# Kernel optimization log

Hardware: AMD Instinct MI355X
Metric: run time of the kernel (lower is better)

Reference implementation:

```python
import jax, jax.numpy as jnp
import numpy as np

EPS = 1e-5  # torch BatchNorm1d default eps


def _bn(x, gamma, beta):
    # training-mode batch norm over axis 0 (biased variance, like torch)
    m = x.mean(axis=0)
    v = x.var(axis=0)
    return (x - m) * jax.lax.rsqrt(v + EPS) * gamma + beta


def setup_inputs() -> dict:
    key = jax.random.key(0)
    ks = jax.random.split(key, 6)
    B, T, D_IN, E, H, D_OUT = 8192, 64, 2, 128, 128, 5
    s = 0.05
    f32 = jnp.float32
    return {
        "inputs": jax.random.normal(ks[0], (B, T, D_IN), f32),
        # input BatchNorm1d(2)
        "in_gamma": jnp.ones((D_IN,), f32),
        "in_beta": jnp.zeros((D_IN,), f32),
        # input embed MLP: Linear(2->128) + BN(128) + ReLU
        "W_emb": jax.random.normal(ks[1], (E, D_IN), f32) * s,
        "b_emb": jnp.zeros((E,), f32),
        "emb_gamma": jnp.ones((E,), f32),
        "emb_beta": jnp.zeros((E,), f32),
        # LSTMCell(128, 128): gate order i, f, g, o
        "W_ih": jax.random.normal(ks[2], (4 * H, E), f32) * s,
        "W_hh": jax.random.normal(ks[3], (4 * H, H), f32) * s,
        "b_ih": jnp.zeros((4 * H,), f32),
        "b_hh": jnp.zeros((4 * H,), f32),
        # output MLP: Linear(128->5) + BN(5), no activation
        "W_out": jax.random.normal(ks[4], (D_OUT, H), f32) * s,
        "b_out": jnp.zeros((D_OUT,), f32),
        "out_gamma": jnp.ones((D_OUT,), f32),
        "out_beta": jnp.zeros((D_OUT,), f32),
    }


def reference(inputs, in_gamma, in_beta, W_emb, b_emb, emb_gamma, emb_beta,
              W_ih, W_hh, b_ih, b_hh, W_out, b_out, out_gamma, out_beta):
    B, T, D = inputs.shape
    H = W_hh.shape[1]
    # input_norm over flattened (B*T, 2)
    x = _bn(inputs.reshape(-1, D), in_gamma, in_beta).reshape(B, T, D)

    h0 = jnp.zeros((B, H), inputs.dtype)
    c0 = jnp.zeros((B, H), inputs.dtype)

    def step(hc, x_t):
        h, c = hc
        # embed: Linear + BN + ReLU (per-step batch stats, as in torch loop)
        e = jax.nn.relu(_bn(x_t @ W_emb.T + b_emb, emb_gamma, emb_beta))
        gates = e @ W_ih.T + b_ih + h @ W_hh.T + b_hh
        i, f, g, o = jnp.split(gates, 4, axis=-1)
        c_new = jax.nn.sigmoid(f) * c + jax.nn.sigmoid(i) * jnp.tanh(g)
        h_new = jax.nn.sigmoid(o) * jnp.tanh(c_new)
        out = _bn(h_new @ W_out.T + b_out, out_gamma, out_beta)
        return (h_new, c_new), out

    (h, c), outs = jax.lax.scan(step, (h0, c0), jnp.swapaxes(x, 0, 1))
    return jnp.swapaxes(outs, 0, 1), (h, c)  # [B, T, 5], ([B,H],[B,H])
```

## Files before the change

### kernel.cpp

```cpp
#include <hip/hip_runtime.h>
#include <hip/hip_bf16.h>

#define BB 8192
#define TT 64
#define L2E 1.44269504088896f

typedef __attribute__((ext_vector_type(8))) short bf16x8;
typedef __attribute__((ext_vector_type(4))) float f32x4;

__device__ __forceinline__ float exp2g(float x) { return __builtin_amdgcn_exp2f(x); }
__device__ __forceinline__ float rcpg(float x)  { return __builtin_amdgcn_rcpf(x); }
__device__ __forceinline__ short f2bf_s(float x) {
  __hip_bfloat16 b = __float2bfloat16(x);
  return *reinterpret_cast<short*>(&b);
}
__device__ __forceinline__ int aidx(int row, int k) {
  return row * 512 + ((((k >> 3) ^ (row & 7))) << 3) + (k & 7);
}

__global__ void prep_kernel(const float* __restrict__ Wih, const float* __restrict__ Whh,
                            const float* __restrict__ bih, const float* __restrict__ bhh,
                            const float* __restrict__ Wout,
                            short* __restrict__ Wcb, short* __restrict__ Woutb,
                            float* __restrict__ bc) {
  int idx = blockIdx.x * 256 + threadIdx.x;
  if (idx < 16384) {
    int l = idx & 63, f = idx >> 6;
    int kt = f >> 5, nt = f & 31;
    int k0 = kt * 32 + ((l >> 4) << 3);
    int col = nt * 16 + (l & 15);
    int gate = col >> 7;
    float s = (gate == 2) ? (2.f * L2E) : (-L2E);
    const float* src = (k0 < 128) ? (Wih + col * 128 + k0) : (Whh + col * 128 + (k0 - 128));
    bf16x8 v;
    #pragma unroll
    for (int e = 0; e < 8; e++) v[e] = f2bf_s(src[e] * s);
    *(bf16x8*)(Wcb + (size_t)idx * 8) = v;
  } else if (idx < 16640) {
    int i2 = idx - 16384;
    int l = i2 & 63, f = i2 >> 6;
    int k0 = f * 32 + ((l >> 4) << 3);
    int col = l & 15;
    bf16x8 v;
    #pragma unroll
    for (int e = 0; e < 8; e++)
      v[e] = (col < 5) ? f2bf_s(Wout[col * 128 + k0 + e]) : (short)0;
    *(bf16x8*)(Woutb + (size_t)i2 * 8) = v;
  } else {
    int i3 = idx - 16640;
    int gate = i3 >> 7;
    float s = (gate == 2) ? (2.f * L2E) : (-L2E);
    bc[i3] = (bih[i3] + bhh[i3]) * s;
  }
}

__global__ void stats_kernel(const float* __restrict__ x, float* __restrict__ stats) {
  int t = blockIdx.x, tid = threadIdx.x;
  float s0=0, s1=0, s2=0, s3=0, s4=0;
  for (int b = tid; b < BB; b += 256) {
    const float* p = x + ((size_t)b * TT + t) * 2;
    float x0 = p[0], x1 = p[1];
    s0 += x0; s1 += x1; s2 += x0*x0; s3 += x0*x1; s4 += x1*x1;
  }
  __shared__ float red[4][5];
  int lane = tid & 63, w = tid >> 6;
  #pragma unroll
  for (int off = 32; off > 0; off >>= 1) {
    s0 += __shfl_down(s0, off); s1 += __shfl_down(s1, off);
    s2 += __shfl_down(s2, off); s3 += __shfl_down(s3, off); s4 += __shfl_down(s4, off);
  }
  if (lane == 0) { red[w][0]=s0; red[w][1]=s1; red[w][2]=s2; red[w][3]=s3; red[w][4]=s4; }
  __syncthreads();
  if (tid < 5) stats[t*5 + tid] = red[0][tid] + red[1][tid] + red[2][tid] + red[3][tid];
}

__global__ void coef_kernel(const float* __restrict__ stats,
                            const float* __restrict__ Wemb, const float* __restrict__ bemb,
                            const float* __restrict__ ing, const float* __restrict__ inb,
                            const float* __restrict__ eg, const float* __restrict__ eb,
                            float* __restrict__ A0, float* __restrict__ A1, float* __restrict__ Ct) {
  __shared__ float st[64][5];
  __shared__ float glob[4];
  int tid = threadIdx.x;
  for (int i = tid; i < 320; i += 128) st[i / 5][i % 5] = stats[i];
  __syncthreads();
  if (tid == 0) {
    float S0=0, S1=0, S00=0, S11=0;
    for (int t = 0; t < 64; t++) { S0+=st[t][0]; S1+=st[t][1]; S00+=st[t][2]; S11+=st[t][4]; }
    float inv_n = 1.f / (float)(BB * TT);
    float M0 = S0*inv_n, M1 = S1*inv_n;
    float V0 = S00*inv_n - M0*M0, V1 = S11*inv_n - M1*M1;
    float P0 = rsqrtf(V0 + 1e-5f) * ing[0];
    float P1 = rsqrtf(V1 + 1e-5f) * ing[1];
    glob[0]=P0; glob[1]=P1; glob[2]=inb[0]-M0*P0; glob[3]=inb[1]-M1*P1;
  }
  __syncthreads();
  float P0=glob[0], P1=glob[1], Q0=glob[2], Q1=glob[3];
  int j = tid;
  float w0 = Wemb[j*2], w1 = Wemb[j*2+1];
  float a0 = P0*w0, a1 = P1*w1;
  float cj = Q0*w0 + Q1*w1 + bemb[j];
  float gam = eg[j], bet = eb[j];
  float invB = 1.f / (float)BB;
  for (int t = 0; t < 64; t++) {
    float m0 = st[t][0]*invB, m1 = st[t][1]*invB;
    float v00 = st[t][2]*invB - m0*m0;
    float v01 = st[t][3]*invB - m0*m1;
    float v11 = st[t][4]*invB - m1*m1;
    float mean = a0*m0 + a1*m1 + cj;
    float var  = a0*a0*v00 + 2.f*a0*a1*v01 + a1*a1*v11;
    float G = rsqrtf(var + 1e-5f) * gam;
    A0[t*128 + j] = G * a0;
    A1[t*128 + j] = G * a1;
    Ct[t*128 + j] = G * cj + (bet - mean * G);
  }
}

__device__ __forceinline__ void write_e(short* acts_s,
                                        const float* __restrict__ A0, const float* __restrict__ A1,
                                        const float* __restrict__ Ct,
                                        int t, int er, int cg, float x0, float x1) {
  const float4 a0a = *(const float4*)(A0 + t*128 + cg*8);
  const float4 a0b = *(const float4*)(A0 + t*128 + cg*8 + 4);
  const float4 a1a = *(const float4*)(A1 + t*128 + cg*8);
  const float4 a1b = *(const float4*)(A1 + t*128 + cg*8 + 4);
  const float4 cta = *(const float4*)(Ct + t*128 + cg*8);
  const float4 ctb = *(const float4*)(Ct + t*128 + cg*8 + 4);
  bf16x8 v;
  v[0] = f2bf_s(fmaxf(fmaf(a0a.x, x0, fmaf(a1a.x, x1, cta.x)), 0.f));
  v[1] = f2bf_s(fmaxf(fmaf(a0a.y, x0, fmaf(a1a.y, x1, cta.y)), 0.f));
  v[2] = f2bf_s(fmaxf(fmaf(a0a.z, x0, fmaf(a1a.z, x1, cta.z)), 0.f));
  v[3] = f2bf_s(fmaxf(fmaf(a0a.w, x0, fmaf(a1a.w, x1, cta.w)), 0.f));
  v[4] = f2bf_s(fmaxf(fmaf(a0b.x, x0, fmaf(a1b.x, x1, ctb.x)), 0.f));
  v[5] = f2bf_s(fmaxf(fmaf(a0b.y, x0, fmaf(a1b.y, x1, ctb.y)), 0.f));
  v[6] = f2bf_s(fmaxf(fmaf(a0b.z, x0, fmaf(a1b.z, x1, ctb.z)), 0.f));
  v[7] = f2bf_s(fmaxf(fmaf(a0b.w, x0, fmaf(a1b.w, x1, ctb.w)), 0.f));
  int gk = (t & 1) * 16 + cg;
  *(bf16x8*)&acts_s[er * 512 + ((gk ^ (er & 7)) << 3)] = v;
}

__launch_bounds__(512, 1)
__global__ void lstm_kernel(const float* __restrict__ x,
                            const float* __restrict__ A0, const float* __restrict__ A1,
                            const float* __restrict__ Ctab,
                            const short* __restrict__ Wcb, const float* __restrict__ bc,
                            const short* __restrict__ Woutb, const float* __restrict__ bout,
                            float* __restrict__ outy, float* __restrict__ hout,
                            float* __restrict__ cout) {
  __shared__ __align__(16) short acts_s[32 * 512];
  __shared__ __align__(16) float xs[32 * 128];

  const int tid  = threadIdx.x;
  const int lane = tid & 63;
  const int w    = tid >> 6;
  const int row0 = blockIdx.x * 32;
  const int cl   = lane & 15;
  const int lq   = lane >> 4;
  const int er   = tid >> 4;
  const int cg   = tid & 15;

  {
    const float4* src = (const float4*)(x + (size_t)row0 * 128);
    float4* dst = (float4*)xs;
    dst[tid]       = src[tid];
    dst[tid + 512] = src[tid + 512];
  }

  float bgs[4];
  #pragma unroll
  for (int g = 0; g < 4; g++) bgs[g] = bc[g * 128 + w * 16 + cl];
  const float bov = (cl < 5) ? bout[cl] : 0.f;

  bf16x8 wreg[8][4];
  {
    const bf16x8* wptr = (const bf16x8*)Wcb;
    #pragma unroll
    for (int kt = 0; kt < 8; kt++)
      #pragma unroll
      for (int g = 0; g < 4; g++)
        wreg[kt][g] = wptr[(size_t)(kt * 32 + g * 8 + w) * 64 + lane];
  }
  bf16x8 wof[4];
  if ((w & 3) == 0) {
    #pragma unroll
    for (int kyt = 0; kyt < 4; kyt++)
      wof[kyt] = *(const bf16x8*)(Woutb + (size_t)(kyt * 64 + lane) * 8);
  }

  __syncthreads();

  write_e(acts_s, A0, A1, Ctab, 0, er, cg, xs[er * 128], xs[er * 128 + 1]);
  {
    bf16x8 z = (bf16x8)0;
    int gk = 32 + 16 + cg;
    *(bf16x8*)&acts_s[er * 512 + ((gk ^ (er & 7)) << 3)] = z;
  }

  f32x4 cstate[2] = {{0.f,0.f,0.f,0.f},{0.f,0.f,0.f,0.f}};
  float hl[2][4];

  #pragma unroll 1
  for (int t = 0; t < TT; t++) {
    __syncthreads();
    const int ebuf = t & 1;
    const int hbuf = (t + 1) & 1;

    if ((w & 3) == 0 && t > 0) {
      int mty = w >> 2;
      int row = mty * 16 + cl;
      f32x4 ya = (f32x4){0.f,0.f,0.f,0.f};
      #pragma unroll
      for (int kyt = 0; kyt < 4; kyt++) {
        int k = 256 + hbuf * 128 + (kyt * 4 + lq) * 8;
        bf16x8 ah = *(const bf16x8*)&acts_s[aidx(row, k)];
        ya = __builtin_amdgcn_mfma_f32_16x16x32_bf16(ah, wof[kyt], ya, 0, 0, 0);
      }
      if (cl < 5) {
        #pragma unroll
        for (int q = 0; q < 4; q++) {
          int brow = row0 + mty * 16 + lq * 4 + q;
          outy[((size_t)brow * TT + (t - 1)) * 5 + cl] = ya[q] + bov;
        }
      }
    }

    f32x4 acc[4][2];
    #pragma unroll
    for (int g = 0; g < 4; g++)
      #pragma unroll
      for (int mt = 0; mt < 2; mt++)
        acc[g][mt] = (f32x4){bgs[g], bgs[g], bgs[g], bgs[g]};

    #pragma unroll
    for (int kt = 0; kt < 8; kt++) {
      int k = (kt < 4) ? (ebuf * 128 + (kt * 4 + lq) * 8)
                       : (256 + hbuf * 128 + ((kt - 4) * 4 + lq) * 8);
      bf16x8 a0 = *(const bf16x8*)&acts_s[aidx(cl, k)];
      bf16x8 a1 = *(const bf16x8*)&acts_s[aidx(16 + cl, k)];
      #pragma unroll
      for (int g = 0; g < 4; g++) {
        acc[g][0] = __builtin_amdgcn_mfma_f32_16x16x32_bf16(a0, wreg[kt][g], acc[g][0], 0, 0, 0);
        acc[g][1] = __builtin_amdgcn_mfma_f32_16x16x32_bf16(a1, wreg[kt][g], acc[g][1], 0, 0, 0);
      }
    }

    #pragma unroll
    for (int mt = 0; mt < 2; mt++) {
      #pragma unroll
      for (int q = 0; q < 4; q++) {
        float Ei = exp2g(acc[0][mt][q]);
        float Ef = exp2g(acc[1][mt][q]);
        float Eg = exp2g(acc[2][mt][q]);
        float Eo = exp2g(acc[3][mt][q]);
        float di = 1.f + Ei, dg = 1.f + Eg;
        float ig = (Eg - 1.f) * rcpg(di * dg);
        float fv = rcpg(1.f + Ef);
        float cn = fmaf(fv, cstate[mt][q], ig);
        cstate[mt][q] = cn;
        float Ec = exp2g(cn * (2.f * L2E));
        float hn = (Ec - 1.f) * rcpg((1.f + Eo) * (1.f + Ec));
        hl[mt][q] = hn;
        int row = mt * 16 + lq * 4 + q;
        int k   = 256 + (t & 1) * 128 + w * 16 + cl;
        acts_s[aidx(row, k)] = f2bf_s(hn);
      }
    }
    if (t < TT - 1)
      write_e(acts_s, A0, A1, Ctab, t + 1, er, cg,
              xs[er * 128 + (t + 1) * 2], xs[er * 128 + (t + 1) * 2 + 1]);
  }

  __syncthreads();
  if ((w & 3) == 0) {
    int mty = w >> 2;
    int row = mty * 16 + cl;
    int hbuf = TT & 1 ? 0 : 1;
    f32x4 ya = (f32x4){0.f,0.f,0.f,0.f};
    #pragma unroll
    for (int kyt = 0; kyt < 4; kyt++) {
      int k = 256 + ((TT - 1) & 1) * 128 + (kyt * 4 + lq) * 8;
      bf16x8 ah = *(const bf16x8*)&acts_s[aidx(row, k)];
      ya = __builtin_amdgcn_mfma_f32_16x16x32_bf16(ah, wof[kyt], ya, 0, 0, 0);
    }
    (void)hbuf;
    if (cl < 5) {
      #pragma unroll
      for (int q = 0; q < 4; q++) {
        int brow = row0 + mty * 16 + lq * 4 + q;
        outy[((size_t)brow * TT + (TT - 1)) * 5 + cl] = ya[q] + bov;
      }
    }
  }

  #pragma unroll
  for (int mt = 0; mt < 2; mt++) {
    #pragma unroll
    for (int q = 0; q < 4; q++) {
      int brow = row0 + mt * 16 + lq * 4 + q;
      int col  = w * 16 + cl;
      hout[(size_t)brow * 128 + col] = hl[mt][q];
      cout[(size_t)brow * 128 + col] = cstate[mt][q];
    }
  }
}

__global__ void ostats_kernel(const float* __restrict__ outy, float* __restrict__ ost) {
  int t = blockIdx.x, tid = threadIdx.x;
  float s[5] = {0,0,0,0,0}, s2[5] = {0,0,0,0,0};
  for (int b = tid; b < BB; b += 256) {
    const float* p = outy + ((size_t)b * TT + t) * 5;
    #pragma unroll
    for (int k = 0; k < 5; k++) { float v = p[k]; s[k] += v; s2[k] += v*v; }
  }
  __shared__ float red[4][10];
  int lane = tid & 63, w = tid >> 6;
  #pragma unroll
  for (int off = 32; off > 0; off >>= 1) {
    #pragma unroll
    for (int k = 0; k < 5; k++) {
      s[k]  += __shfl_down(s[k], off);
      s2[k] += __shfl_down(s2[k], off);
    }
  }
  if (lane == 0) {
    #pragma unroll
    for (int k = 0; k < 5; k++) { red[w][k] = s[k]; red[w][5+k] = s2[k]; }
  }
  __syncthreads();
  if (tid < 10) ost[t*10 + tid] = red[0][tid]+red[1][tid]+red[2][tid]+red[3][tid];
}

__global__ void onorm_kernel(float* __restrict__ outy, const float* __restrict__ ost,
                             const float* __restrict__ og, const float* __restrict__ ob) {
  const int N = BB*TT*5;
  const float invB = 1.f / (float)BB;
  for (int i = blockIdx.x * 256 + threadIdx.x; i < N; i += gridDim.x * 256) {
    int k = i % 5;
    int t = (i / 5) % TT;
    float m = ost[t*10 + k] * invB;
    float v = ost[t*10 + 5 + k] * invB - m*m;
    outy[i] = (outy[i] - m) * rsqrtf(v + 1e-5f) * og[k] + ob[k];
  }
}

extern "C" void kernel_launch(void* const* d_in, const int* in_sizes, int n_in,
                              void* d_out, int out_size, void* d_ws, size_t ws_size,
                              hipStream_t stream) {
  const float* xin  = (const float*)d_in[0];
  const float* ing  = (const float*)d_in[1];
  const float* inb  = (const float*)d_in[2];
  const float* Wemb = (const float*)d_in[3];
  const float* bemb = (const float*)d_in[4];
  const float* eg   = (const float*)d_in[5];
  const float* eb   = (const float*)d_in[6];
  const float* Wih  = (const float*)d_in[7];
  const float* Whh  = (const float*)d_in[8];
  const float* bih  = (const float*)d_in[9];
  const float* bhh  = (const float*)d_in[10];
  const float* Wout = (const float*)d_in[11];
  const float* bout = (const float*)d_in[12];
  const float* og   = (const float*)d_in[13];
  const float* ob   = (const float*)d_in[14];

  float* ws    = (float*)d_ws;
  float* stats = ws;
  float* A0    = ws + 1024;
  float* A1    = ws + 9216;
  float* Ct    = ws + 17408;
  float* bc    = ws + 25600;
  short* Wcb   = (short*)(ws + 26624);
  short* Woutb = (short*)(ws + 92160);
  float* ost   = ws + 93184;

  float* outy = (float*)d_out;
  float* hout = outy + (size_t)BB * TT * 5;
  float* cout = hout + (size_t)BB * 128;

  prep_kernel <<<67, 256, 0, stream>>>(Wih, Whh, bih, bhh, Wout, Wcb, Woutb, bc);
  stats_kernel<<<64, 256, 0, stream>>>(xin, stats);
  coef_kernel <<<1, 128, 0, stream>>>(stats, Wemb, bemb, ing, inb, eg, eb, A0, A1, Ct);
  lstm_kernel <<<256, 512, 0, stream>>>(xin, A0, A1, Ct, Wcb, bc, Woutb, bout,
                                        outy, hout, cout);
  ostats_kernel<<<64, 256, 0, stream>>>(outy, ost);
  onorm_kernel <<<2048, 256, 0, stream>>>(outy, ost, og, ob);
}
```

Before: 248.4 us.

## Merge prep/stats kernels, prefetch embed coefs, split ostats, precompute norm scales

Merges the weight-prep and input-stats kernels into one launch. In the LSTM loop, the next step's embedding coefficients are loaded before the matmul to hide global latency, and the MFMA section runs at raised wave priority. Output stats are split four ways per timestep for more parallelism. The output norm precomputes per-(t,k) scale and shift in shared memory and applies a single fma. Prefetching adds register pressure to a kernel already running at one block per CU.

```diff
diff --git a/kernel.cpp b/kernel.cpp
--- a/kernel.cpp
+++ b/kernel.cpp
@@ -18,60 +18,61 @@
   return row * 512 + ((((k >> 3) ^ (row & 7))) << 3) + (k & 7);
 }
 
-__global__ void prep_kernel(const float* __restrict__ Wih, const float* __restrict__ Whh,
-                            const float* __restrict__ bih, const float* __restrict__ bhh,
-                            const float* __restrict__ Wout,
-                            short* __restrict__ Wcb, short* __restrict__ Woutb,
-                            float* __restrict__ bc) {
-  int idx = blockIdx.x * 256 + threadIdx.x;
-  if (idx < 16384) {
-    int l = idx & 63, f = idx >> 6;
-    int kt = f >> 5, nt = f & 31;
-    int k0 = kt * 32 + ((l >> 4) << 3);
-    int col = nt * 16 + (l & 15);
-    int gate = col >> 7;
-    float s = (gate == 2) ? (2.f * L2E) : (-L2E);
-    const float* src = (k0 < 128) ? (Wih + col * 128 + k0) : (Whh + col * 128 + (k0 - 128));
-    bf16x8 v;
-    #pragma unroll
-    for (int e = 0; e < 8; e++) v[e] = f2bf_s(src[e] * s);
-    *(bf16x8*)(Wcb + (size_t)idx * 8) = v;
-  } else if (idx < 16640) {
-    int i2 = idx - 16384;
-    int l = i2 & 63, f = i2 >> 6;
-    int k0 = f * 32 + ((l >> 4) << 3);
-    int col = l & 15;
-    bf16x8 v;
-    #pragma unroll
-    for (int e = 0; e < 8; e++)
-      v[e] = (col < 5) ? f2bf_s(Wout[col * 128 + k0 + e]) : (short)0;
-    *(bf16x8*)(Woutb + (size_t)i2 * 8) = v;
+__global__ void prep_stats_kernel(const float* __restrict__ Wih, const float* __restrict__ Whh,
+                                  const float* __restrict__ bih, const float* __restrict__ bhh,
+                                  const float* __restrict__ Wout,
+                                  short* __restrict__ Wcb, short* __restrict__ Woutb,
+                                  float* __restrict__ bc,
+                                  const float* __restrict__ x, float* __restrict__ stats) {
+  if (blockIdx.x < 67) {
+    int idx = blockIdx.x * 256 + threadIdx.x;
+    if (idx < 16384) {
+      int l = idx & 63, f = idx >> 6;
+      int kt = f >> 5, nt = f & 31;
+      int k0 = kt * 32 + ((l >> 4) << 3);
+      int col = nt * 16 + (l & 15);
+      int gate = col >> 7;
+      float s = (gate == 2) ? (2.f * L2E) : (-L2E);
+      const float* src = (k0 < 128) ? (Wih + col * 128 + k0) : (Whh + col * 128 + (k0 - 128));
+      bf16x8 v;
+      #pragma unroll
+      for (int e = 0; e < 8; e++) v[e] = f2bf_s(src[e] * s);
+      *(bf16x8*)(Wcb + (size_t)idx * 8) = v;
+    } else if (idx < 16640) {
+      int i2 = idx - 16384;
+      int l = i2 & 63, f = i2 >> 6;
+      int k0 = f * 32 + ((l >> 4) << 3);
+      int col = l & 15;
+      bf16x8 v;
+      #pragma unroll
+      for (int e = 0; e < 8; e++)
+        v[e] = (col < 5) ? f2bf_s(Wout[col * 128 + k0 + e]) : (short)0;
+      *(bf16x8*)(Woutb + (size_t)i2 * 8) = v;
+    } else {
+      int i3 = idx - 16640;
+      int gate = i3 >> 7;
+      float s = (gate == 2) ? (2.f * L2E) : (-L2E);
+      bc[i3] = (bih[i3] + bhh[i3]) * s;
+    }
   } else {
-    int i3 = idx - 16640;
-    int gate = i3 >> 7;
-    float s = (gate == 2) ? (2.f * L2E) : (-L2E);
-    bc[i3] = (bih[i3] + bhh[i3]) * s;
-  }
-}
-
-__global__ void stats_kernel(const float* __restrict__ x, float* __restrict__ stats) {
-  int t = blockIdx.x, tid = threadIdx.x;
-  float s0=0, s1=0, s2=0, s3=0, s4=0;
-  for (int b = tid; b < BB; b += 256) {
-    const float* p = x + ((size_t)b * TT + t) * 2;
-    float x0 = p[0], x1 = p[1];
-    s0 += x0; s1 += x1; s2 += x0*x0; s3 += x0*x1; s4 += x1*x1;
-  }
-  __shared__ float red[4][5];
-  int lane = tid & 63, w = tid >> 6;
-  #pragma unroll
-  for (int off = 32; off > 0; off >>= 1) {
-    s0 += __shfl_down(s0, off); s1 += __shfl_down(s1, off);
-    s2 += __shfl_down(s2, off); s3 += __shfl_down(s3, off); s4 += __shfl_down(s4, off);
-  }
-  if (lane == 0) { red[w][0]=s0; red[w][1]=s1; red[w][2]=s2; red[w][3]=s3; red[w][4]=s4; }
-  __syncthreads();
-  if (tid < 5) stats[t*5 + tid] = red[0][tid] + red[1][tid] + red[2][tid] + red[3][tid];
+    int t = blockIdx.x - 67, tid = threadIdx.x;
+    float s0=0, s1=0, s2=0, s3=0, s4=0;
+    for (int b = tid; b < BB; b += 256) {
+      const float* p = x + ((size_t)b * TT + t) * 2;
+      float x0 = p[0], x1 = p[1];
+      s0 += x0; s1 += x1; s2 += x0*x0; s3 += x0*x1; s4 += x1*x1;
+    }
+    __shared__ float red[4][5];
+    int lane = tid & 63, w = tid >> 6;
+    #pragma unroll
+    for (int off = 32; off > 0; off >>= 1) {
+      s0 += __shfl_down(s0, off); s1 += __shfl_down(s1, off);
+      s2 += __shfl_down(s2, off); s3 += __shfl_down(s3, off); s4 += __shfl_down(s4, off);
+    }
+    if (lane == 0) { red[w][0]=s0; red[w][1]=s1; red[w][2]=s2; red[w][3]=s3; red[w][4]=s4; }
+    __syncthreads();
+    if (tid < 5) stats[t*5 + tid] = red[0][tid] + red[1][tid] + red[2][tid] + red[3][tid];
+  }
 }
 
 __global__ void coef_kernel(const float* __restrict__ stats,
@@ -116,16 +117,10 @@
   }
 }
 
-__device__ __forceinline__ void write_e(short* acts_s,
-                                        const float* __restrict__ A0, const float* __restrict__ A1,
-                                        const float* __restrict__ Ct,
-                                        int t, int er, int cg, float x0, float x1) {
-  const float4 a0a = *(const float4*)(A0 + t*128 + cg*8);
-  const float4 a0b = *(const float4*)(A0 + t*128 + cg*8 + 4);
-  const float4 a1a = *(const float4*)(A1 + t*128 + cg*8);
-  const float4 a1b = *(const float4*)(A1 + t*128 + cg*8 + 4);
-  const float4 cta = *(const float4*)(Ct + t*128 + cg*8);
-  const float4 ctb = *(const float4*)(Ct + t*128 + cg*8 + 4);
+__device__ __forceinline__ void write_e_reg(short* acts_s, int t, int er, int cg,
+                                            float x0, float x1,
+                                            float4 a0a, float4 a0b, float4 a1a, float4 a1b,
+                                            float4 cta, float4 ctb) {
   bf16x8 v;
   v[0] = f2bf_s(fmaxf(fmaf(a0a.x, x0, fmaf(a1a.x, x1, cta.x)), 0.f));
   v[1] = f2bf_s(fmaxf(fmaf(a0a.y, x0, fmaf(a1a.y, x1, cta.y)), 0.f));
@@ -189,8 +184,14 @@
 
   __syncthreads();
 
-  write_e(acts_s, A0, A1, Ctab, 0, er, cg, xs[er * 128], xs[er * 128 + 1]);
   {
+    const float* a0p = A0 + cg*8;
+    const float* a1p = A1 + cg*8;
+    const float* ccp = Ctab + cg*8;
+    write_e_reg(acts_s, 0, er, cg, xs[er*128], xs[er*128+1],
+                *(const float4*)a0p, *(const float4*)(a0p+4),
+                *(const float4*)a1p, *(const float4*)(a1p+4),
+                *(const float4*)ccp, *(const float4*)(ccp+4));
     bf16x8 z = (bf16x8)0;
     int gk = 32 + 16 + cg;
     *(bf16x8*)&acts_s[er * 512 + ((gk ^ (er & 7)) << 3)] = z;
@@ -204,6 +205,17 @@
     __syncthreads();
     const int ebuf = t & 1;
     const int hbuf = (t + 1) & 1;
+    const bool do_e = (t < TT - 1);
+
+    float4 ta0a, ta0b, ta1a, ta1b, tcta, tctb;
+    if (do_e) {
+      const float* a0p = A0 + (t + 1) * 128 + cg * 8;
+      const float* a1p = A1 + (t + 1) * 128 + cg * 8;
+      const float* ccp = Ctab + (t + 1) * 128 + cg * 8;
+      ta0a = *(const float4*)a0p;  ta0b = *(const float4*)(a0p + 4);
+      ta1a = *(const float4*)a1p;  ta1b = *(const float4*)(a1p + 4);
+      tcta = *(const float4*)ccp;  tctb = *(const float4*)(ccp + 4);
+    }
 
     if ((w & 3) == 0 && t > 0) {
       int mty = w >> 2;
@@ -231,6 +243,7 @@
       for (int mt = 0; mt < 2; mt++)
         acc[g][mt] = (f32x4){bgs[g], bgs[g], bgs[g], bgs[g]};
 
+    __builtin_amdgcn_s_setprio(1);
     #pragma unroll
     for (int kt = 0; kt < 8; kt++) {
       int k = (kt < 4) ? (ebuf * 128 + (kt * 4 + lq) * 8)
@@ -243,6 +256,7 @@
         acc[g][1] = __builtin_amdgcn_mfma_f32_16x16x32_bf16(a1, wreg[kt][g], acc[g][1], 0, 0, 0);
       }
     }
+    __builtin_amdgcn_s_setprio(0);
 
     #pragma unroll
     for (int mt = 0; mt < 2; mt++) {
@@ -265,16 +279,16 @@
         acts_s[aidx(row, k)] = f2bf_s(hn);
       }
     }
-    if (t < TT - 1)
-      write_e(acts_s, A0, A1, Ctab, t + 1, er, cg,
-              xs[er * 128 + (t + 1) * 2], xs[er * 128 + (t + 1) * 2 + 1]);
+    if (do_e)
+      write_e_reg(acts_s, t + 1, er, cg,
+                  xs[er * 128 + (t + 1) * 2], xs[er * 128 + (t + 1) * 2 + 1],
+                  ta0a, ta0b, ta1a, ta1b, tcta, tctb);
   }
 
   __syncthreads();
   if ((w & 3) == 0) {
     int mty = w >> 2;
     int row = mty * 16 + cl;
-    int hbuf = TT & 1 ? 0 : 1;
     f32x4 ya = (f32x4){0.f,0.f,0.f,0.f};
     #pragma unroll
     for (int kyt = 0; kyt < 4; kyt++) {
@@ -282,7 +296,6 @@
       bf16x8 ah = *(const bf16x8*)&acts_s[aidx(row, k)];
       ya = __builtin_amdgcn_mfma_f32_16x16x32_bf16(ah, wof[kyt], ya, 0, 0, 0);
     }
-    (void)hbuf;
     if (cl < 5) {
       #pragma unroll
       for (int q = 0; q < 4; q++) {
@@ -304,10 +317,12 @@
   }
 }
 
-__global__ void ostats_kernel(const float* __restrict__ outy, float* __restrict__ ost) {
-  int t = blockIdx.x, tid = threadIdx.x;
+__global__ void ostats_kernel(const float* __restrict__ outy, float* __restrict__ ostp) {
+  int t = blockIdx.x >> 2, part = blockIdx.x & 3;
+  int tid = threadIdx.x;
   float s[5] = {0,0,0,0,0}, s2[5] = {0,0,0,0,0};
-  for (int b = tid; b < BB; b += 256) {
+  int b0 = part * 2048;
+  for (int b = b0 + tid; b < b0 + 2048; b += 256) {
     const float* p = outy + ((size_t)b * TT + t) * 5;
     #pragma unroll
     for (int k = 0; k < 5; k++) { float v = p[k]; s[k] += v; s2[k] += v*v; }
@@ -327,19 +342,28 @@
     for (int k = 0; k < 5; k++) { red[w][k] = s[k]; red[w][5+k] = s2[k]; }
   }
   __syncthreads();
-  if (tid < 10) ost[t*10 + tid] = red[0][tid]+red[1][tid]+red[2][tid]+red[3][tid];
-}
-
-__global__ void onorm_kernel(float* __restrict__ outy, const float* __restrict__ ost,
+  if (tid < 10) ostp[blockIdx.x * 10 + tid] = red[0][tid]+red[1][tid]+red[2][tid]+red[3][tid];
+}
+
+__global__ void onorm_kernel(float* __restrict__ outy, const float* __restrict__ ostp,
                              const float* __restrict__ og, const float* __restrict__ ob) {
-  const int N = BB*TT*5;
+  __shared__ float sc[320], sh[320];
+  int tid = threadIdx.x;
   const float invB = 1.f / (float)BB;
-  for (int i = blockIdx.x * 256 + threadIdx.x; i < N; i += gridDim.x * 256) {
-    int k = i % 5;
-    int t = (i / 5) % TT;
-    float m = ost[t*10 + k] * invB;
-    float v = ost[t*10 + 5 + k] * invB - m*m;
-    outy[i] = (outy[i] - m) * rsqrtf(v + 1e-5f) * og[k] + ob[k];
+  for (int i = tid; i < 320; i += 256) {
+    int t = i / 5, k = i - t * 5;
+    float m  = (ostp[(t*4+0)*10+k]   + ostp[(t*4+1)*10+k]   + ostp[(t*4+2)*10+k]   + ostp[(t*4+3)*10+k]) * invB;
+    float s2 = (ostp[(t*4+0)*10+5+k] + ostp[(t*4+1)*10+5+k] + ostp[(t*4+2)*10+5+k] + ostp[(t*4+3)*10+5+k]) * invB;
+    float v = s2 - m * m;
+    float scale = rsqrtf(v + 1e-5f) * og[k];
+    sc[i] = scale;
+    sh[i] = ob[k] - m * scale;
+  }
+  __syncthreads();
+  const int N = BB * TT * 5;
+  for (int i = blockIdx.x * 256 + tid; i < N; i += gridDim.x * 256) {
+    int j = i % 320;
+    outy[i] = fmaf(outy[i], sc[j], sh[j]);
   }
 }
 
@@ -370,17 +394,17 @@
   float* bc    = ws + 25600;
   short* Wcb   = (short*)(ws + 26624);
   short* Woutb = (short*)(ws + 92160);
-  float* ost   = ws + 93184;
+  float* ostp  = ws + 93184;
 
   float* outy = (float*)d_out;
   float* hout = outy + (size_t)BB * TT * 5;
   float* cout = hout + (size_t)BB * 128;
 
-  prep_kernel <<<67, 256, 0, stream>>>(Wih, Whh, bih, bhh, Wout, Wcb, Woutb, bc);
-  stats_kernel<<<64, 256, 0, stream>>>(xin, stats);
+  prep_stats_kernel<<<131, 256, 0, stream>>>(Wih, Whh, bih, bhh, Wout, Wcb, Woutb, bc,
+                                             xin, stats);
   coef_kernel <<<1, 128, 0, stream>>>(stats, Wemb, bemb, ing, inb, eg, eb, A0, A1, Ct);
   lstm_kernel <<<256, 512, 0, stream>>>(xin, A0, A1, Ct, Wcb, bc, Woutb, bout,
                                         outy, hout, cout);
-  ostats_kernel<<<64, 256, 0, stream>>>(outy, ost);
-  onorm_kernel <<<2048, 256, 0, stream>>>(outy, ost, og, ob);
-}
+  ostats_kernel<<<256, 256, 0, stream>>>(outy, ostp);
+  onorm_kernel <<<1024, 256, 0, stream>>>(outy, ostp, og, ob);
+}
```

Measured after the change: 265.8 us. 7.0% more time.
